# Kernel optimization log

Hardware: AMD Instinct MI355X
Metric: run time of the kernel (lower is better)

Reference implementation:

```python
import jax, jax.numpy as jnp
import numpy as np

PERI_IDX = np.array([0, 1, 2, 3, 5, 6, 7, 8])  # non-center taps of the 3x3 window


def _extract_patches(x, stride, padding):
    # x: [B,C,H,W] -> patches [B,C,9,Hout,Wout], tap k = di*3+dj (row-major), matching F.unfold.
    B, C, H, W = x.shape
    Hout = (H + 2 * padding - 3) // stride + 1
    Wout = (W + 2 * padding - 3) // stride + 1
    xp = jnp.pad(x, ((0, 0), (0, 0), (padding, padding), (padding, padding)))
    taps = [xp[:, :, di:di + (Hout - 1) * stride + 1:stride, dj:dj + (Wout - 1) * stride + 1:stride]
            for di in range(3) for dj in range(3)]
    return jnp.stack(taps, axis=2)  # [B,C,9,Hout,Wout]


def setup_inputs() -> dict:
    key = jax.random.key(0)
    k1, k2, k3, k4 = jax.random.split(key, 4)
    B, C, O, H, W = 8, 64, 64, 128, 128
    x = jax.random.normal(k1, (B, C, H, W), dtype=jnp.float32)
    core = jax.random.normal(k2, (O, C, 1, 1), dtype=jnp.float32) * (1.0 / np.sqrt(C))
    periphery = jax.random.uniform(k3, (8,), dtype=jnp.float32, minval=-0.1, maxval=0.1)
    threshold = jnp.array([0.1], dtype=jnp.float32)
    scale = jnp.array([10.0], dtype=jnp.float32)
    return {"x": x, "core": core, "periphery": periphery, "threshold": threshold,
            "scale": scale, "stride": 1, "padding": 1}


def reference(x, core, periphery, threshold, scale, stride, padding):
    B, C, H, W = x.shape
    O = core.shape[0]
    patches = _extract_patches(x, stride, padding)           # [B,C,9,Ho,Wo]
    center = patches[:, :, 4]                                 # [B,C,Ho,Wo]
    # per-pixel variance-like routing statistic over channels and taps
    div = jnp.sum((patches - center[:, :, None]) ** 2, axis=(1, 2))  # [B,Ho,Wo]
    m_hard = jax.nn.sigmoid((div - threshold[0]) * scale[0]) > 0.5   # [B,Ho,Wo] bool
    w = core.reshape(O, C)
    # path 0 (low variance): 1x1 conv on the center pixel
    zero_out = jnp.einsum('bchw,oc->bohw', center, w)
    # path 1 (high variance): periphery-weighted sum then 1x1 conv
    agg = jnp.einsum('bckhw,k->bchw', patches[:, :, PERI_IDX], periphery)
    one_out = jnp.einsum('bchw,oc->bohw', agg, w)
    return jnp.where(m_hard[:, None], one_out, zero_out)
```

## Files before the change

kernel.cpp:

```cpp
#include <hip/hip_runtime.h>
#include <hip/hip_bf16.h>

constexpr int Bc = 8;
constexpr int Cc = 64;
constexpr int Oc = 64;
constexpr int Hc = 128;
constexpr int Wc = 128;
constexpr int HWc = Hc * Wc;
constexpr int CP = 72;

typedef __attribute__((ext_vector_type(8))) short short8;
typedef __attribute__((ext_vector_type(4))) short short4v;
typedef __attribute__((ext_vector_type(4))) float floatx4;

__device__ __forceinline__ int swz(int w, int c) {
    return ((((c >> 3) ^ (w >> 2)) & 7) << 3) | (c & 7);
}

__device__ __forceinline__ short f2bf(float f) {
    __hip_bfloat16 h = __float2bfloat16(f);
    return *reinterpret_cast<short*>(&h);
}

__global__ __launch_bounds__(512, 4) void spconv_kernel(
    const float* __restrict__ x, const float* __restrict__ core,
    const float* __restrict__ peri, const float* __restrict__ thr,
    const float* __restrict__ scl, float* __restrict__ out)
{
    __shared__ __hip_bfloat16 s_selT[Wc][CP];
    __shared__ __hip_bfloat16 s_core[Oc][CP];
    __shared__ float s_divp[16][Wc];
    __shared__ float s_msk[Wc];

    const int tid = threadIdx.x;
    const int wg  = tid & 31;
    const int cg  = tid >> 5;
    const int w0  = wg * 4;
    const int c0  = cg * 4;
    const int b   = blockIdx.x >> 7;
    const int h   = blockIdx.x & (Hc - 1);

    #pragma unroll
    for (int i = 0; i < 2; ++i) {
        const int idx = (i * 512 + tid) * 4;
        const floatx4 cv = *(const floatx4*)&core[idx];
        short4v cv16 = { f2bf(cv.x), f2bf(cv.y), f2bf(cv.z), f2bf(cv.w) };
        *(short4v*)&s_core[idx >> 6][idx & 63] = cv16;
    }

    const float* xb = x + (size_t)b * Cc * HWc + (size_t)h * Wc;
    const bool hm = (h > 0), hp = (h < Hc - 1);

    float p[8];
    #pragma unroll
    for (int k = 0; k < 8; ++k) p[k] = peri[k];

    float div4[4] = {0.f, 0.f, 0.f, 0.f};
    float aggv[4][4];
    const floatx4 zero4 = {0.f, 0.f, 0.f, 0.f};

    #pragma unroll
    for (int ch = 0; ch < 4; ++ch) {
        const float* row = xb + (size_t)(c0 + ch) * HWc;
        const floatx4 tc = hm ? *(const floatx4*)(row - Wc + w0) : zero4;
        const floatx4 mc =      *(const floatx4*)(row      + w0);
        const floatx4 bc = hp ? *(const floatx4*)(row + Wc + w0) : zero4;

        float tl = __shfl_up(tc.w, 1, 32),  tr = __shfl_down(tc.x, 1, 32);
        float ml = __shfl_up(mc.w, 1, 32),  mr = __shfl_down(mc.x, 1, 32);
        float bl = __shfl_up(bc.w, 1, 32),  br = __shfl_down(bc.x, 1, 32);
        if (wg == 0)  { tl = 0.f; ml = 0.f; bl = 0.f; }
        if (wg == 31) { tr = 0.f; mr = 0.f; br = 0.f; }

        const float top[6] = {tl, tc.x, tc.y, tc.z, tc.w, tr};
        const float mid[6] = {ml, mc.x, mc.y, mc.z, mc.w, mr};
        const float bot[6] = {bl, bc.x, bc.y, bc.z, bc.w, br};

        #pragma unroll
        for (int j = 0; j < 4; ++j) {
            const float t4 = mid[j + 1];
            float a = p[0] * top[j];
            a = fmaf(p[1], top[j + 1], a);
            a = fmaf(p[2], top[j + 2], a);
            a = fmaf(p[3], mid[j],     a);
            a = fmaf(p[4], mid[j + 2], a);
            a = fmaf(p[5], bot[j],     a);
            a = fmaf(p[6], bot[j + 1], a);
            a = fmaf(p[7], bot[j + 2], a);
            aggv[ch][j] = a;

            float s = div4[j], d;
            d = top[j]     - t4; s = fmaf(d, d, s);
            d = top[j + 1] - t4; s = fmaf(d, d, s);
            d = top[j + 2] - t4; s = fmaf(d, d, s);
            d = mid[j]     - t4; s = fmaf(d, d, s);
            d = mid[j + 2] - t4; s = fmaf(d, d, s);
            d = bot[j]     - t4; s = fmaf(d, d, s);
            d = bot[j + 1] - t4; s = fmaf(d, d, s);
            d = bot[j + 2] - t4; s = fmaf(d, d, s);
            div4[j] = s;
        }
    }

    #pragma unroll
    for (int j = 0; j < 4; ++j) {
        short4v av = { f2bf(aggv[0][j]), f2bf(aggv[1][j]),
                       f2bf(aggv[2][j]), f2bf(aggv[3][j]) };
        *(short4v*)&s_selT[w0 + j][swz(w0 + j, c0)] = av;
    }
    floatx4 dv4 = {div4[0], div4[1], div4[2], div4[3]};
    *(floatx4*)&s_divp[cg][w0] = dv4;
    __syncthreads();

    if (tid < Wc) {
        float dv = 0.f;
        #pragma unroll
        for (int g = 0; g < 16; ++g) dv += s_divp[g][tid];
        s_msk[tid] = (((dv - thr[0]) * scl[0]) > 0.f) ? 1.f : 0.f;
    }
    __syncthreads();

    #pragma unroll
    for (int i = 0; i < 16; ++i) {
        const int idx = i * 512 + tid;
        const int ww  = idx & (Wc - 1);
        const int c   = idx >> 7;
        if (s_msk[ww] == 0.f)
            s_selT[ww][swz(ww, c)] = __float2bfloat16(xb[(size_t)c * HWc + ww]);
    }
    __syncthreads();

    const int lane = tid & 63;
    const int wid  = tid >> 6;
    const int o0   = (wid & 3) * 16;
    const int wh   = wid >> 2;
    const int n    = lane & 15;
    const int quad = lane >> 4;

    const short8 a0 = *(const short8*)&s_core[o0 + n][quad * 8];
    const short8 a1 = *(const short8*)&s_core[o0 + n][quad * 8 + 32];

    float* outb = out + ((size_t)(b * Oc) * Hc + h) * Wc;

    #pragma unroll
    for (int t = 0; t < 4; ++t) {
        const int wq = (wh * 4 + t) * 16 + n;
        const short8 b0 = *(const short8*)&s_selT[wq][swz(wq, quad * 8)];
        const short8 b1 = *(const short8*)&s_selT[wq][swz(wq, quad * 8 + 32)];
        floatx4 acc = {0.f, 0.f, 0.f, 0.f};
        acc = __builtin_amdgcn_mfma_f32_16x16x32_bf16(a0, b0, acc, 0, 0, 0);
        acc = __builtin_amdgcn_mfma_f32_16x16x32_bf16(a1, b1, acc, 0, 0, 0);
        #pragma unroll
        for (int r = 0; r < 4; ++r) {
            const int o = o0 + quad * 4 + r;
            outb[(size_t)o * HWc + wq] = acc[r];
        }
    }
}

extern "C" void kernel_launch(void* const* d_in, const int* in_sizes, int n_in,
                              void* d_out, int out_size, void* d_ws, size_t ws_size,
                              hipStream_t stream) {
    const float* x    = (const float*)d_in[0];
    const float* core = (const float*)d_in[1];
    const float* peri = (const float*)d_in[2];
    const float* thr  = (const float*)d_in[3];
    const float* scl  = (const float*)d_in[4];
    float* out = (float*)d_out;

    spconv_kernel<<<dim3(Bc * Hc), dim3(512), 0, stream>>>(
        x, core, peri, thr, scl, out);
}
```

Baseline: 110.4 us.

## Halve block size, double channels per thread, fuse mask and center fill

The block shrinks from 512 to 256 threads. Each thread now processes 8 channels in two chunks of 4, and each wave computes 16 output channels across all 128 columns in 8 MFMA tiles. The separate mask pass, its shared array and one barrier are removed: thread pairs sum the divergence partials per pixel and, for low-variance pixels, write that pixel's 32 center channels straight into shared memory. The aim is fewer barriers and more blocks resident per CU. The cost is a serial per-thread fill loop with divergent, less coalesced global loads.

```diff
diff --git a/kernel.cpp b/kernel.cpp
--- a/kernel.cpp
+++ b/kernel.cpp
@@ -22,27 +22,31 @@
     return *reinterpret_cast<short*>(&h);
 }
 
-__global__ __launch_bounds__(512, 4) void spconv_kernel(
+__global__ __launch_bounds__(256, 5) void spconv_kernel(
     const float* __restrict__ x, const float* __restrict__ core,
     const float* __restrict__ peri, const float* __restrict__ thr,
     const float* __restrict__ scl, float* __restrict__ out)
 {
     __shared__ __hip_bfloat16 s_selT[Wc][CP];
     __shared__ __hip_bfloat16 s_core[Oc][CP];
-    __shared__ float s_divp[16][Wc];
-    __shared__ float s_msk[Wc];
+    __shared__ float s_divp[8][Wc];
 
     const int tid = threadIdx.x;
     const int wg  = tid & 31;
     const int cg  = tid >> 5;
     const int w0  = wg * 4;
-    const int c0  = cg * 4;
+    const int c0  = cg * 8;
     const int b   = blockIdx.x >> 7;
     const int h   = blockIdx.x & (Hc - 1);
 
+    const float thr0 = thr[0], scl0 = scl[0];
+    float p[8];
     #pragma unroll
-    for (int i = 0; i < 2; ++i) {
-        const int idx = (i * 512 + tid) * 4;
+    for (int k = 0; k < 8; ++k) p[k] = peri[k];
+
+    #pragma unroll
+    for (int i = 0; i < 4; ++i) {
+        const int idx = (i * 256 + tid) * 4;
         const floatx4 cv = *(const floatx4*)&core[idx];
         short4v cv16 = { f2bf(cv.x), f2bf(cv.y), f2bf(cv.z), f2bf(cv.w) };
         *(short4v*)&s_core[idx >> 6][idx & 63] = cv16;
@@ -50,90 +54,82 @@
 
     const float* xb = x + (size_t)b * Cc * HWc + (size_t)h * Wc;
     const bool hm = (h > 0), hp = (h < Hc - 1);
-
-    float p[8];
-    #pragma unroll
-    for (int k = 0; k < 8; ++k) p[k] = peri[k];
+    const floatx4 zero4 = {0.f, 0.f, 0.f, 0.f};
 
     float div4[4] = {0.f, 0.f, 0.f, 0.f};
-    float aggv[4][4];
-    const floatx4 zero4 = {0.f, 0.f, 0.f, 0.f};
 
     #pragma unroll
-    for (int ch = 0; ch < 4; ++ch) {
-        const float* row = xb + (size_t)(c0 + ch) * HWc;
-        const floatx4 tc = hm ? *(const floatx4*)(row - Wc + w0) : zero4;
-        const floatx4 mc =      *(const floatx4*)(row      + w0);
-        const floatx4 bc = hp ? *(const floatx4*)(row + Wc + w0) : zero4;
+    for (int chunk = 0; chunk < 2; ++chunk) {
+        float aggv[4][4];
+        #pragma unroll
+        for (int ch = 0; ch < 4; ++ch) {
+            const float* row = xb + (size_t)(c0 + chunk * 4 + ch) * HWc;
+            const floatx4 tc = hm ? *(const floatx4*)(row - Wc + w0) : zero4;
+            const floatx4 mc =      *(const floatx4*)(row      + w0);
+            const floatx4 bc = hp ? *(const floatx4*)(row + Wc + w0) : zero4;
 
-        float tl = __shfl_up(tc.w, 1, 32),  tr = __shfl_down(tc.x, 1, 32);
-        float ml = __shfl_up(mc.w, 1, 32),  mr = __shfl_down(mc.x, 1, 32);
-        float bl = __shfl_up(bc.w, 1, 32),  br = __shfl_down(bc.x, 1, 32);
-        if (wg == 0)  { tl = 0.f; ml = 0.f; bl = 0.f; }
-        if (wg == 31) { tr = 0.f; mr = 0.f; br = 0.f; }
+            float tl = __shfl_up(tc.w, 1, 32),  tr = __shfl_down(tc.x, 1, 32);
+            float ml = __shfl_up(mc.w, 1, 32),  mr = __shfl_down(mc.x, 1, 32);
+            float bl = __shfl_up(bc.w, 1, 32),  br = __shfl_down(bc.x, 1, 32);
+            if (wg == 0)  { tl = 0.f; ml = 0.f; bl = 0.f; }
+            if (wg == 31) { tr = 0.f; mr = 0.f; br = 0.f; }
 
-        const float top[6] = {tl, tc.x, tc.y, tc.z, tc.w, tr};
-        const float mid[6] = {ml, mc.x, mc.y, mc.z, mc.w, mr};
-        const float bot[6] = {bl, bc.x, bc.y, bc.z, bc.w, br};
+            const float top[6] = {tl, tc.x, tc.y, tc.z, tc.w, tr};
+            const float mid[6] = {ml, mc.x, mc.y, mc.z, mc.w, mr};
+            const float bot[6] = {bl, bc.x, bc.y, bc.z, bc.w, br};
 
+            #pragma unroll
+            for (int j = 0; j < 4; ++j) {
+                const float t4 = mid[j + 1];
+                float a = p[0] * top[j];
+                a = fmaf(p[1], top[j + 1], a);
+                a = fmaf(p[2], top[j + 2], a);
+                a = fmaf(p[3], mid[j],     a);
+                a = fmaf(p[4], mid[j + 2], a);
+                a = fmaf(p[5], bot[j],     a);
+                a = fmaf(p[6], bot[j + 1], a);
+                a = fmaf(p[7], bot[j + 2], a);
+                aggv[ch][j] = a;
+
+                float s = div4[j], d;
+                d = top[j]     - t4; s = fmaf(d, d, s);
+                d = top[j + 1] - t4; s = fmaf(d, d, s);
+                d = top[j + 2] - t4; s = fmaf(d, d, s);
+                d = mid[j]     - t4; s = fmaf(d, d, s);
+                d = mid[j + 2] - t4; s = fmaf(d, d, s);
+                d = bot[j]     - t4; s = fmaf(d, d, s);
+                d = bot[j + 1] - t4; s = fmaf(d, d, s);
+                d = bot[j + 2] - t4; s = fmaf(d, d, s);
+                div4[j] = s;
+            }
+        }
         #pragma unroll
         for (int j = 0; j < 4; ++j) {
-            const float t4 = mid[j + 1];
-            float a = p[0] * top[j];
-            a = fmaf(p[1], top[j + 1], a);
-            a = fmaf(p[2], top[j + 2], a);
-            a = fmaf(p[3], mid[j],     a);
-            a = fmaf(p[4], mid[j + 2], a);
-            a = fmaf(p[5], bot[j],     a);
-            a = fmaf(p[6], bot[j + 1], a);
-            a = fmaf(p[7], bot[j + 2], a);
-            aggv[ch][j] = a;
-
-            float s = div4[j], d;
-            d = top[j]     - t4; s = fmaf(d, d, s);
-            d = top[j + 1] - t4; s = fmaf(d, d, s);
-            d = top[j + 2] - t4; s = fmaf(d, d, s);
-            d = mid[j]     - t4; s = fmaf(d, d, s);
-            d = mid[j + 2] - t4; s = fmaf(d, d, s);
-            d = bot[j]     - t4; s = fmaf(d, d, s);
-            d = bot[j + 1] - t4; s = fmaf(d, d, s);
-            d = bot[j + 2] - t4; s = fmaf(d, d, s);
-            div4[j] = s;
+            short4v av = { f2bf(aggv[0][j]), f2bf(aggv[1][j]),
+                           f2bf(aggv[2][j]), f2bf(aggv[3][j]) };
+            *(short4v*)&s_selT[w0 + j][swz(w0 + j, c0 + chunk * 4)] = av;
         }
-    }
-
-    #pragma unroll
-    for (int j = 0; j < 4; ++j) {
-        short4v av = { f2bf(aggv[0][j]), f2bf(aggv[1][j]),
-                       f2bf(aggv[2][j]), f2bf(aggv[3][j]) };
-        *(short4v*)&s_selT[w0 + j][swz(w0 + j, c0)] = av;
     }
     floatx4 dv4 = {div4[0], div4[1], div4[2], div4[3]};
     *(floatx4*)&s_divp[cg][w0] = dv4;
     __syncthreads();
 
-    if (tid < Wc) {
+    {
+        const int wf  = tid >> 1;
+        const int cb  = (tid & 1) * 32;
         float dv = 0.f;
         #pragma unroll
-        for (int g = 0; g < 16; ++g) dv += s_divp[g][tid];
-        s_msk[tid] = (((dv - thr[0]) * scl[0]) > 0.f) ? 1.f : 0.f;
-    }
-    __syncthreads();
-
-    #pragma unroll
-    for (int i = 0; i < 16; ++i) {
-        const int idx = i * 512 + tid;
-        const int ww  = idx & (Wc - 1);
-        const int c   = idx >> 7;
-        if (s_msk[ww] == 0.f)
-            s_selT[ww][swz(ww, c)] = __float2bfloat16(xb[(size_t)c * HWc + ww]);
+        for (int g = 0; g < 8; ++g) dv += s_divp[g][wf];
+        if (((dv - thr0) * scl0) <= 0.f) {
+            for (int c = cb; c < cb + 32; ++c)
+                s_selT[wf][swz(wf, c)] = __float2bfloat16(xb[(size_t)c * HWc + wf]);
+        }
     }
     __syncthreads();
 
     const int lane = tid & 63;
     const int wid  = tid >> 6;
-    const int o0   = (wid & 3) * 16;
-    const int wh   = wid >> 2;
+    const int o0   = wid * 16;
     const int n    = lane & 15;
     const int quad = lane >> 4;
 
@@ -143,8 +139,8 @@
     float* outb = out + ((size_t)(b * Oc) * Hc + h) * Wc;
 
     #pragma unroll
-    for (int t = 0; t < 4; ++t) {
-        const int wq = (wh * 4 + t) * 16 + n;
+    for (int t = 0; t < 8; ++t) {
+        const int wq = t * 16 + n;
         const short8 b0 = *(const short8*)&s_selT[wq][swz(wq, quad * 8)];
         const short8 b1 = *(const short8*)&s_selT[wq][swz(wq, quad * 8 + 32)];
         floatx4 acc = {0.f, 0.f, 0.f, 0.f};
@@ -168,6 +164,6 @@
     const float* scl  = (const float*)d_in[4];
     float* out = (float*)d_out;
 
-    spconv_kernel<<<dim3(Bc * Hc), dim3(512), 0, stream>>>(
+    spconv_kernel<<<dim3(Bc * Hc), dim3(256), 0, stream>>>(
         x, core, peri, thr, scl, out);
 }
```

New measurement: 223.8 us. +102.8%, slower.
